# Performance work log

Hardware: AMD Instinct MI355X
Metric: run time of the kernel (lower is better)

The kernel has to match this reference:

```python
import jax, jax.numpy as jnp
import numpy as np

L, D, N = 4096, 1024, 16  # seq_len, d_model, hiddens_per_input


def setup_inputs() -> dict:
    key = jax.random.key(0)
    ks = jax.random.split(key, 9)
    x = jax.random.normal(ks[0], (L, D), dtype=jnp.float32)
    # Delta param (pre-softplus); softplus(Delta) > 0 is the discretization step
    Delta = jax.random.normal(ks[1], (D,), dtype=jnp.float32)
    # A stored as (re, im); default scheme uses A_re = -1 (stable), theta in [0, 2pi)
    A_re = -(0.5 + 0.5 * jax.random.uniform(ks[2], (D, N), dtype=jnp.float32))
    A_im = jax.random.uniform(ks[3], (D, N), dtype=jnp.float32) * 2.0 * jnp.pi
    scale = 1.0 / jnp.sqrt(jnp.float32(D))  # matrix_init: randn / sqrt(shape[0])
    B_re = jax.random.normal(ks[4], (D, N), dtype=jnp.float32) * scale
    B_im = jax.random.normal(ks[5], (D, N), dtype=jnp.float32) * scale
    C_re = jax.random.normal(ks[6], (D, N), dtype=jnp.float32) * scale
    C_im = jax.random.normal(ks[7], (D, N), dtype=jnp.float32) * scale
    D_param = jax.random.normal(ks[8], (D,), dtype=jnp.float32) * scale
    return {"x": x, "Delta": Delta, "A_re": A_re, "A_im": A_im,
            "B_re": B_re, "B_im": B_im, "C_re": C_re, "C_im": C_im,
            "D_param": D_param}


def _binary_operator_diag(q_i, q_j):
    """Associative op for diagonal linear recurrence h_j = A_j h_{j-1} + b_j."""
    A_i, b_i = q_i
    A_j, b_j = q_j
    return (A_j * A_i, A_j * b_i + b_j)


def reference(x, Delta, A_re, A_im, B_re, B_im, C_re, C_im, D_param):
    Bc = B_re + 1j * B_im                      # (D, N) complex
    Cc = C_re + 1j * C_im                      # (D, N) complex
    Ac = A_re + 1j * A_im                      # (D, N) complex
    dt = jax.nn.softplus(Delta)                # (D,)
    # shared_Delta=True branch: Lambda = exp(dt[:, None] * A), repeated over L
    Lam = jnp.exp(dt[:, None] * Ac)            # (D, N) complex
    Lambda_elements = jnp.broadcast_to(Lam[None, :, :], (x.shape[0], *Lam.shape))
    # Bu = einsum('D, D N, L D -> L D N', dt, B, x)
    Bu_elements = jnp.einsum('D,DN,LD->LDN', dt.astype(Bc.dtype), Bc,
                             x.astype(Bc.dtype))
    _, hidden_states = jax.lax.associative_scan(
        _binary_operator_diag, (Lambda_elements, Bu_elements))  # (L, D, N)
    out = jnp.einsum('LDN,DN->LD', hidden_states, Cc) + D_param[None, :] * x
    return out.real
```

## Files before the change

kernel.cpp:

```cpp
#include <hip/hip_runtime.h>
#include <math.h>

constexpr int L   = 4096;
constexpr int D   = 1024;
constexpr int CPB = 4;
constexpr int NB  = D / CPB;
constexpr int NCB = 128;
constexpr int T   = L / NCB;
constexpr int NT  = 1024;
constexpr int N   = 16;
constexpr int PAD = 65;

typedef float v2 __attribute__((ext_vector_type(2)));

__device__ __forceinline__ float softplus_f(float v) {
    return fmaxf(v, 0.0f) + log1pf(expf(-fabsf(v)));
}

__device__ __forceinline__ void lam_fast(float ar, float ai, float dt,
                                         float& lr, float& li) {
    float e = __expf(ar * dt);
    float s, c;
    __sincosf(ai * dt, &s, &c);
    lr = e * c;
    li = e * s;
}

__device__ __forceinline__ v2 vfma(v2 a, v2 b, v2 c) {
    return __builtin_elementwise_fma(a, b, c);
}

__global__ __launch_bounds__(NT, 4) void k_fused(
    const float* __restrict__ x,
    const float* __restrict__ Delta,
    const float* __restrict__ A_re, const float* __restrict__ A_im,
    const float* __restrict__ B_re, const float* __restrict__ B_im,
    const float* __restrict__ C_re, const float* __restrict__ C_im,
    const float* __restrict__ Dp,
    float* __restrict__ out)
{
    __shared__ float  xs[T * 512];
    __shared__ float2 sums[NCB * PAD];
    __shared__ float2 tot[16 * 64];

    const int b  = blockIdx.x;
    const int d0 = (b & 7) * 128 + (b >> 3) * 4;
    const int t  = threadIdx.x;

    const int h  = t & 1;
    const int dd = (t >> 1) & 3;
    const int ct = t >> 3;
    const int d  = d0 + dd;

    {
        const int rs = t & 7;
        float4 v[4];
        #pragma unroll
        for (int k = 0; k < 4; ++k) {
            int l = ct * T + rs * 4 + k;
            v[k] = *(const float4*)(x + (size_t)l * D + d0);
        }
        #pragma unroll
        for (int k = 0; k < 4; ++k)
            *(float4*)&xs[(rs * 4 + k) * 512 + ct * 4] = v[k];
    }

    const float dt = softplus_f(Delta[d]);

    v2 LR[4], LI[4];
    {
        const int base = d * N + h * 8;
        float4 a0 = *(const float4*)(A_re + base);
        float4 a1 = *(const float4*)(A_re + base + 4);
        float4 m0 = *(const float4*)(A_im + base);
        float4 m1 = *(const float4*)(A_im + base + 4);
        const float ar[8] = {a0.x, a0.y, a0.z, a0.w, a1.x, a1.y, a1.z, a1.w};
        const float ai[8] = {m0.x, m0.y, m0.z, m0.w, m1.x, m1.y, m1.z, m1.w};
        #pragma unroll
        for (int p = 0; p < 4; ++p) {
            float lr0, li0, lr1, li1;
            lam_fast(ar[2 * p], ai[2 * p], dt, lr0, li0);
            lam_fast(ar[2 * p + 1], ai[2 * p + 1], dt, lr1, li1);
            LR[p] = (v2){lr0, lr1};
            LI[p] = (v2){li0, li1};
        }
    }

    asm volatile("s_waitcnt vmcnt(0) lgkmcnt(0)" ::: "memory");

    v2 GR[4] = {(v2)0, (v2)0, (v2)0, (v2)0};
    v2 GI[4] = {(v2)0, (v2)0, (v2)0, (v2)0};
    #pragma unroll 4
    for (int i = 0; i < T; ++i) {
        float xv = xs[i * 512 + ct * 4 + dd];
        v2 XV = (v2){xv, xv};
        #pragma unroll
        for (int p = 0; p < 4; ++p) {
            v2 t2 = vfma(-LI[p], GI[p], XV);
            v2 nr = vfma(LR[p], GR[p], t2);
            GI[p] = vfma(LR[p], GI[p], LI[p] * GR[p]);
            GR[p] = nr;
        }
    }
    {
        float2* sp = &sums[ct * PAD + dd * 16 + h * 8];
        #pragma unroll
        for (int p = 0; p < 4; ++p) {
            sp[2 * p]     = make_float2(GR[p].x, GI[p].x);
            sp[2 * p + 1] = make_float2(GR[p].y, GI[p].y);
        }
    }

    const int lane = t & 63;
    const int w    = t >> 6;
    float l32r, l32i;
    {
        const int dd2 = lane >> 4, n2 = lane & 15;
        const int d2  = d0 + dd2;
        const float dt2 = softplus_f(Delta[d2]);
        lam_fast(A_re[d2 * N + n2], A_im[d2 * N + n2], dt2, l32r, l32i);
        #pragma unroll
        for (int k = 0; k < 5; ++k) {
            float nr = l32r * l32r - l32i * l32i;
            l32i = 2.0f * l32r * l32i;
            l32r = nr;
        }
    }

    asm volatile("s_waitcnt lgkmcnt(0)" ::: "memory");

    {
        float cr = 0.0f, ci = 0.0f;
        #pragma unroll
        for (int k = 0; k < 8; ++k) {
            const int idx = (w * 8 + k) * PAD + lane;
            float2 sv = sums[idx];
            sums[idx] = make_float2(cr, ci);
            float nr = fmaf(l32r, cr, fmaf(-l32i, ci, sv.x));
            ci = fmaf(l32r, ci, fmaf(l32i, cr, sv.y));
            cr = nr;
        }
        tot[w * 64 + lane] = make_float2(cr, ci);
    }

    float4 b0, b1, e0, e1, f0, f1, g0, g1;
    {
        const int base = d * N + h * 8;
        b0 = *(const float4*)(B_re + base);
        b1 = *(const float4*)(B_re + base + 4);
        e0 = *(const float4*)(B_im + base);
        e1 = *(const float4*)(B_im + base + 4);
        f0 = *(const float4*)(C_re + base);
        f1 = *(const float4*)(C_re + base + 4);
        g0 = *(const float4*)(C_im + base);
        g1 = *(const float4*)(C_im + base + 4);
    }
    const float dpv = Dp[d];

    __syncthreads();

    if (t < 64) {
        float rr = l32r, ri = l32i;
        #pragma unroll
        for (int k = 0; k < 3; ++k) {
            float nr = rr * rr - ri * ri;
            ri = 2.0f * rr * ri;
            rr = nr;
        }
        float cr = 0.0f, ci = 0.0f;
        #pragma unroll
        for (int u = 0; u < 16; ++u) {
            float2 sv = tot[u * 64 + t];
            tot[u * 64 + t] = make_float2(cr, ci);
            float nr = fmaf(rr, cr, fmaf(-ri, ci, sv.x));
            ci = fmaf(rr, ci, fmaf(ri, cr, sv.y));
            cr = nr;
        }
    }

    __syncthreads();

    {
        float2 g = tot[w * 64 + lane];
        float gr = g.x, gi = g.y;
        #pragma unroll
        for (int k = 0; k < 8; ++k) {
            const int idx = (w * 8 + k) * PAD + lane;
            float2 p = sums[idx];
            sums[idx] = make_float2(gr + p.x, gi + p.y);
            float nr = l32r * gr - l32i * gi;
            gi = fmaf(l32r, gi, l32i * gr);
            gr = nr;
        }
    }

    v2 CR[4], CI[4];
    {
        const float br[8] = {b0.x, b0.y, b0.z, b0.w, b1.x, b1.y, b1.z, b1.w};
        const float bi[8] = {e0.x, e0.y, e0.z, e0.w, e1.x, e1.y, e1.z, e1.w};
        const float cr[8] = {f0.x, f0.y, f0.z, f0.w, f1.x, f1.y, f1.z, f1.w};
        const float ci[8] = {g0.x, g0.y, g0.z, g0.w, g1.x, g1.y, g1.z, g1.w};
        #pragma unroll
        for (int p = 0; p < 4; ++p) {
            CR[p] = (v2){dt * (cr[2*p] * br[2*p] - ci[2*p] * bi[2*p]),
                         dt * (cr[2*p+1] * br[2*p+1] - ci[2*p+1] * bi[2*p+1])};
            CI[p] = (v2){dt * (cr[2*p] * bi[2*p] + ci[2*p] * br[2*p]),
                         dt * (cr[2*p+1] * bi[2*p+1] + ci[2*p+1] * br[2*p+1])};
        }
    }

    asm volatile("s_waitcnt lgkmcnt(0)" ::: "memory");

    {
        const float2* cp = &sums[ct * PAD + dd * 16 + h * 8];
        #pragma unroll
        for (int p = 0; p < 4; ++p) {
            float2 c0 = cp[2 * p], c1 = cp[2 * p + 1];
            GR[p] = (v2){c0.x, c1.x};
            GI[p] = (v2){c0.y, c1.y};
        }
    }
    const float dsel0 = h ? 0.0f : dpv;
    const float dsel1 = h ? dpv  : 0.0f;
    #pragma unroll
    for (int ob = 0; ob < T / 8; ++ob) {
        float P0[4], P1[4];
        #pragma unroll
        for (int ib = 0; ib < 4; ++ib) {
            #pragma unroll
            for (int u = 0; u < 2; ++u) {
                int i = ob * 8 + ib * 2 + u;
                float xv = xs[i * 512 + ct * 4 + dd];
                v2 XV = (v2){xv, xv};
                v2 ACC = (v2)0;
                #pragma unroll
                for (int p = 0; p < 4; ++p) {
                    v2 t2 = vfma(-LI[p], GI[p], XV);
                    v2 nr = vfma(LR[p], GR[p], t2);
                    GI[p] = vfma(LR[p], GI[p], LI[p] * GR[p]);
                    GR[p] = nr;
                    ACC = vfma(CR[p], GR[p], ACC);
                    ACC = vfma(-CI[p], GI[p], ACC);
                }
                float ap = ACC.x + ACC.y;
                ap = fmaf(u == 0 ? dsel0 : dsel1, xv, ap);
                if (u == 0) P0[ib] = ap; else P1[ib] = ap;
            }
        }
        float Vh[4];
        #pragma unroll
        for (int ib = 0; ib < 4; ++ib) {
            float mine  = h ? P1[ib] : P0[ib];
            float other = h ? P0[ib] : P1[ib];
            Vh[ib] = mine + __shfl_xor(other, 1);
        }
        float f[4];
        f[dd]     = Vh[dd];
        f[dd ^ 1] = __shfl_xor(Vh[dd ^ 1], 2);
        f[dd ^ 2] = __shfl_xor(Vh[dd ^ 2], 4);
        f[dd ^ 3] = __shfl_xor(Vh[dd ^ 3], 6);
        int row = ct * T + ob * 8 + dd * 2 + h;
        *(float4*)(out + (size_t)row * D + d0) =
            make_float4(f[0], f[1], f[2], f[3]);
    }
}

extern "C" void kernel_launch(void* const* d_in, const int* in_sizes, int n_in,
                              void* d_out, int out_size, void* d_ws, size_t ws_size,
                              hipStream_t stream) {
    const float* x     = (const float*)d_in[0];
    const float* Delta = (const float*)d_in[1];
    const float* A_re  = (const float*)d_in[2];
    const float* A_im  = (const float*)d_in[3];
    const float* B_re  = (const float*)d_in[4];
    const float* B_im  = (const float*)d_in[5];
    const float* C_re  = (const float*)d_in[6];
    const float* C_im  = (const float*)d_in[7];
    const float* Dp    = (const float*)d_in[8];
    float* out = (float*)d_out;

    k_fused<<<NB, NT, 0, stream>>>(x, Delta, A_re, A_im, B_re, B_im,
                                   C_re, C_im, Dp, out);
}
```

Baseline: 124.8 us.

## Split sequence into segments across blocks with cooperative grid sync for carries

```diff
diff --git a/kernel.cpp b/kernel.cpp
--- a/kernel.cpp
+++ b/kernel.cpp
@@ -1,15 +1,22 @@
 #include <hip/hip_runtime.h>
+#include <hip/hip_cooperative_groups.h>
 #include <math.h>
 
-constexpr int L   = 4096;
-constexpr int D   = 1024;
-constexpr int CPB = 4;
-constexpr int NB  = D / CPB;
-constexpr int NCB = 128;
-constexpr int T   = L / NCB;
-constexpr int NT  = 1024;
-constexpr int N   = 16;
-constexpr int PAD = 65;
+namespace cgrp = cooperative_groups;
+
+constexpr int L    = 4096;
+constexpr int D    = 1024;
+constexpr int N    = 16;
+constexpr int CPB  = 16;
+constexpr int NCG  = D / CPB;
+constexpr int NSEG = 4;
+constexpr int LSEG = L / NSEG;
+constexpr int NB   = NCG * NSEG;
+constexpr int NT   = 1024;
+constexpr int NCH  = 32;
+constexpr int T    = LSEG / NCH;
+constexpr int NST  = CPB * N;
+constexpr int SSTR = NST + 1;
 
 typedef float v2 __attribute__((ext_vector_type(2)));
 
@@ -37,34 +44,37 @@
     const float* __restrict__ B_re, const float* __restrict__ B_im,
     const float* __restrict__ C_re, const float* __restrict__ C_im,
     const float* __restrict__ Dp,
-    float* __restrict__ out)
+    float* __restrict__ out,
+    float2* __restrict__ sb, int two_sync)
 {
-    __shared__ float  xs[T * 512];
-    __shared__ float2 sums[NCB * PAD];
-    __shared__ float2 tot[16 * 64];
-
-    const int b  = blockIdx.x;
-    const int d0 = (b & 7) * 128 + (b >> 3) * 4;
-    const int t  = threadIdx.x;
+    __shared__ float  xs[LSEG * CPB];
+    __shared__ float2 sums[NCH * SSTR];
+    __shared__ float2 tot[4 * NST];
+
+    cgrp::grid_group grid = cgrp::this_grid();
+
+    const int blk = blockIdx.x;
+    const int cgi = blk & (NCG - 1);
+    const int seg = blk >> 6;
+    const int l0  = seg * LSEG;
+    const int c0  = cgi * CPB;
+    const int t   = threadIdx.x;
+
+    {
+        const int q = t & 3, r = t >> 2;
+        float4 v[4];
+        #pragma unroll
+        for (int k = 0; k < 4; ++k)
+            v[k] = *(const float4*)(x + (size_t)(l0 + r + 256 * k) * D + c0 + q * 4);
+        #pragma unroll
+        for (int k = 0; k < 4; ++k)
+            *(float4*)&xs[(r + 256 * k) * CPB + q * 4] = v[k];
+    }
 
     const int h  = t & 1;
-    const int dd = (t >> 1) & 3;
-    const int ct = t >> 3;
-    const int d  = d0 + dd;
-
-    {
-        const int rs = t & 7;
-        float4 v[4];
-        #pragma unroll
-        for (int k = 0; k < 4; ++k) {
-            int l = ct * T + rs * 4 + k;
-            v[k] = *(const float4*)(x + (size_t)l * D + d0);
-        }
-        #pragma unroll
-        for (int k = 0; k < 4; ++k)
-            *(float4*)&xs[(rs * 4 + k) * 512 + ct * 4] = v[k];
-    }
-
+    const int dd = (t >> 1) & 15;
+    const int ct = t >> 5;
+    const int d  = c0 + dd;
     const float dt = softplus_f(Delta[d]);
 
     v2 LR[4], LI[4];
@@ -85,14 +95,13 @@
             LI[p] = (v2){li0, li1};
         }
     }
-
-    asm volatile("s_waitcnt vmcnt(0) lgkmcnt(0)" ::: "memory");
+    __syncthreads();
 
     v2 GR[4] = {(v2)0, (v2)0, (v2)0, (v2)0};
     v2 GI[4] = {(v2)0, (v2)0, (v2)0, (v2)0};
     #pragma unroll 4
     for (int i = 0; i < T; ++i) {
-        float xv = xs[i * 512 + ct * 4 + dd];
+        float xv = xs[(ct * T + i) * CPB + dd];
         v2 XV = (v2){xv, xv};
         #pragma unroll
         for (int p = 0; p < 4; ++p) {
@@ -102,23 +111,24 @@
             GR[p] = nr;
         }
     }
-    {
-        float2* sp = &sums[ct * PAD + dd * 16 + h * 8];
-        #pragma unroll
-        for (int p = 0; p < 4; ++p) {
-            sp[2 * p]     = make_float2(GR[p].x, GI[p].x);
-            sp[2 * p + 1] = make_float2(GR[p].y, GI[p].y);
-        }
+    #pragma unroll
+    for (int p = 0; p < 4; ++p) {
+        const int s0 = (h * 8 + 2 * p) * CPB + dd;
+        sums[ct * SSTR + s0]       = make_float2(GR[p].x, GI[p].x);
+        sums[ct * SSTR + s0 + CPB] = make_float2(GR[p].y, GI[p].y);
     }
 
     const int lane = t & 63;
     const int w    = t >> 6;
+    const int SL   = w & 3;
+    const int WG   = w >> 2;
+    const int s    = SL * 64 + lane;
     float l32r, l32i;
     {
-        const int dd2 = lane >> 4, n2 = lane & 15;
-        const int d2  = d0 + dd2;
+        const int sdd = s & 15, sn = s >> 4;
+        const int d2 = c0 + sdd;
         const float dt2 = softplus_f(Delta[d2]);
-        lam_fast(A_re[d2 * N + n2], A_im[d2 * N + n2], dt2, l32r, l32i);
+        lam_fast(A_re[d2 * N + sn], A_im[d2 * N + sn], dt2, l32r, l32i);
         #pragma unroll
         for (int k = 0; k < 5; ++k) {
             float nr = l32r * l32r - l32i * l32i;
@@ -126,40 +136,39 @@
             l32r = nr;
         }
     }
-
-    asm volatile("s_waitcnt lgkmcnt(0)" ::: "memory");
+    __syncthreads();
 
     {
         float cr = 0.0f, ci = 0.0f;
         #pragma unroll
         for (int k = 0; k < 8; ++k) {
-            const int idx = (w * 8 + k) * PAD + lane;
+            const int idx = (WG * 8 + k) * SSTR + s;
             float2 sv = sums[idx];
             sums[idx] = make_float2(cr, ci);
             float nr = fmaf(l32r, cr, fmaf(-l32i, ci, sv.x));
             ci = fmaf(l32r, ci, fmaf(l32i, cr, sv.y));
             cr = nr;
         }
-        tot[w * 64 + lane] = make_float2(cr, ci);
-    }
-
-    float4 b0, b1, e0, e1, f0, f1, g0, g1;
+        tot[WG * NST + s] = make_float2(cr, ci);
+    }
+
+    float4 pb0, pb1, pe0, pe1, pf0, pf1, pg0, pg1;
     {
         const int base = d * N + h * 8;
-        b0 = *(const float4*)(B_re + base);
-        b1 = *(const float4*)(B_re + base + 4);
-        e0 = *(const float4*)(B_im + base);
-        e1 = *(const float4*)(B_im + base + 4);
-        f0 = *(const float4*)(C_re + base);
-        f1 = *(const float4*)(C_re + base + 4);
-        g0 = *(const float4*)(C_im + base);
-        g1 = *(const float4*)(C_im + base + 4);
+        pb0 = *(const float4*)(B_re + base);
+        pb1 = *(const float4*)(B_re + base + 4);
+        pe0 = *(const float4*)(B_im + base);
+        pe1 = *(const float4*)(B_im + base + 4);
+        pf0 = *(const float4*)(C_re + base);
+        pf1 = *(const float4*)(C_re + base + 4);
+        pg0 = *(const float4*)(C_im + base);
+        pg1 = *(const float4*)(C_im + base + 4);
     }
     const float dpv = Dp[d];
 
     __syncthreads();
 
-    if (t < 64) {
+    if (w < 4) {
         float rr = l32r, ri = l32i;
         #pragma unroll
         for (int k = 0; k < 3; ++k) {
@@ -169,37 +178,74 @@
         }
         float cr = 0.0f, ci = 0.0f;
         #pragma unroll
-        for (int u = 0; u < 16; ++u) {
-            float2 sv = tot[u * 64 + t];
-            tot[u * 64 + t] = make_float2(cr, ci);
+        for (int u = 0; u < 4; ++u) {
+            const int idx = u * NST + s;
+            float2 sv = tot[idx];
+            tot[idx] = make_float2(cr, ci);
             float nr = fmaf(rr, cr, fmaf(-ri, ci, sv.x));
             ci = fmaf(rr, ci, fmaf(ri, cr, sv.y));
             cr = nr;
         }
-    }
-
-    __syncthreads();
-
-    {
-        float2 g = tot[w * 64 + lane];
-        float gr = g.x, gi = g.y;
+        if (seg != NSEG - 1)
+            sb[(seg * NCG + cgi) * NST + s] = make_float2(cr, ci);
+    }
+    __syncthreads();
+    __threadfence();
+    grid.sync();
+    __threadfence();
+
+    float Cr = 0.0f, Ci = 0.0f;
+    if (seg > 0) {
+        float g1r = l32r, g1i = l32i;
+        #pragma unroll
+        for (int k = 0; k < 5; ++k) {
+            float nr = g1r * g1r - g1i * g1i;
+            g1i = 2.0f * g1r * g1i;
+            g1r = nr;
+        }
+        for (int j = 0; j < seg; ++j) {
+            float2 sv = sb[(j * NCG + cgi) * NST + s];
+            float nr = fmaf(g1r, Cr, fmaf(-g1i, Ci, sv.x));
+            Ci = fmaf(g1r, Ci, fmaf(g1i, Cr, sv.y));
+            Cr = nr;
+        }
+    }
+    if (two_sync) grid.sync();
+
+    {
+        float rr = l32r, ri = l32i;
+        #pragma unroll
+        for (int k = 0; k < 3; ++k) {
+            float nr = rr * rr - ri * ri;
+            ri = 2.0f * rr * ri;
+            rr = nr;
+        }
+        float pr = 1.0f, pi = 0.0f;
+        for (int k = 0; k < WG; ++k) {
+            float nr = pr * rr - pi * ri;
+            pi = fmaf(pr, ri, pi * rr);
+            pr = nr;
+        }
+        float2 g = tot[WG * NST + s];
+        float cr = fmaf(pr, Cr, fmaf(-pi, Ci, g.x));
+        float ci = fmaf(pr, Ci, fmaf(pi, Cr, g.y));
         #pragma unroll
         for (int k = 0; k < 8; ++k) {
-            const int idx = (w * 8 + k) * PAD + lane;
+            const int idx = (WG * 8 + k) * SSTR + s;
             float2 p = sums[idx];
-            sums[idx] = make_float2(gr + p.x, gi + p.y);
-            float nr = l32r * gr - l32i * gi;
-            gi = fmaf(l32r, gi, l32i * gr);
-            gr = nr;
+            sums[idx] = make_float2(cr + p.x, ci + p.y);
+            float nr = l32r * cr - l32i * ci;
+            ci = fmaf(l32r, ci, l32i * cr);
+            cr = nr;
         }
     }
 
     v2 CR[4], CI[4];
     {
-        const float br[8] = {b0.x, b0.y, b0.z, b0.w, b1.x, b1.y, b1.z, b1.w};
-        const float bi[8] = {e0.x, e0.y, e0.z, e0.w, e1.x, e1.y, e1.z, e1.w};
-        const float cr[8] = {f0.x, f0.y, f0.z, f0.w, f1.x, f1.y, f1.z, f1.w};
-        const float ci[8] = {g0.x, g0.y, g0.z, g0.w, g1.x, g1.y, g1.z, g1.w};
+        const float br[8] = {pb0.x, pb0.y, pb0.z, pb0.w, pb1.x, pb1.y, pb1.z, pb1.w};
+        const float bi[8] = {pe0.x, pe0.y, pe0.z, pe0.w, pe1.x, pe1.y, pe1.z, pe1.w};
+        const float cr[8] = {pf0.x, pf0.y, pf0.z, pf0.w, pf1.x, pf1.y, pf1.z, pf1.w};
+        const float ci[8] = {pg0.x, pg0.y, pg0.z, pg0.w, pg1.x, pg1.y, pg1.z, pg1.w};
         #pragma unroll
         for (int p = 0; p < 4; ++p) {
             CR[p] = (v2){dt * (cr[2*p] * br[2*p] - ci[2*p] * bi[2*p]),
@@ -208,20 +254,20 @@
                          dt * (cr[2*p+1] * bi[2*p+1] + ci[2*p+1] * br[2*p+1])};
         }
     }
-
-    asm volatile("s_waitcnt lgkmcnt(0)" ::: "memory");
-
-    {
-        const float2* cp = &sums[ct * PAD + dd * 16 + h * 8];
-        #pragma unroll
-        for (int p = 0; p < 4; ++p) {
-            float2 c0 = cp[2 * p], c1 = cp[2 * p + 1];
-            GR[p] = (v2){c0.x, c1.x};
-            GI[p] = (v2){c0.y, c1.y};
-        }
+    __syncthreads();
+
+    #pragma unroll
+    for (int p = 0; p < 4; ++p) {
+        const int s0 = (h * 8 + 2 * p) * CPB + dd;
+        float2 c0v = sums[ct * SSTR + s0];
+        float2 c1v = sums[ct * SSTR + s0 + CPB];
+        GR[p] = (v2){c0v.x, c1v.x};
+        GI[p] = (v2){c0v.y, c1v.y};
     }
     const float dsel0 = h ? 0.0f : dpv;
     const float dsel1 = h ? dpv  : 0.0f;
+    const int r0 = dd & 3;
+    const int cb = c0 + (dd >> 2) * 4;
     #pragma unroll
     for (int ob = 0; ob < T / 8; ++ob) {
         float P0[4], P1[4];
@@ -230,7 +276,7 @@
             #pragma unroll
             for (int u = 0; u < 2; ++u) {
                 int i = ob * 8 + ib * 2 + u;
-                float xv = xs[i * 512 + ct * 4 + dd];
+                float xv = xs[(ct * T + i) * CPB + dd];
                 v2 XV = (v2){xv, xv};
                 v2 ACC = (v2)0;
                 #pragma unroll
@@ -255,12 +301,12 @@
             Vh[ib] = mine + __shfl_xor(other, 1);
         }
         float f[4];
-        f[dd]     = Vh[dd];
-        f[dd ^ 1] = __shfl_xor(Vh[dd ^ 1], 2);
-        f[dd ^ 2] = __shfl_xor(Vh[dd ^ 2], 4);
-        f[dd ^ 3] = __shfl_xor(Vh[dd ^ 3], 6);
-        int row = ct * T + ob * 8 + dd * 2 + h;
-        *(float4*)(out + (size_t)row * D + d0) =
+        f[r0]     = Vh[r0];
+        f[r0 ^ 1] = __shfl_xor(Vh[r0 ^ 1], 2);
+        f[r0 ^ 2] = __shfl_xor(Vh[r0 ^ 2], 4);
+        f[r0 ^ 3] = __shfl_xor(Vh[r0 ^ 3], 6);
+        int row = l0 + ct * T + ob * 8 + r0 * 2 + h;
+        *(float4*)(out + (size_t)row * D + cb) =
             make_float4(f[0], f[1], f[2], f[3]);
     }
 }
@@ -279,6 +325,18 @@
     const float* Dp    = (const float*)d_in[8];
     float* out = (float*)d_out;
 
-    k_fused<<<NB, NT, 0, stream>>>(x, Delta, A_re, A_im, B_re, B_im,
-                                   C_re, C_im, Dp, out);
-}
+    const size_t need = sizeof(float2) * (size_t)NSEG * NCG * NST;
+    float2* sb;
+    int two_sync;
+    if (d_ws != nullptr && ws_size >= need) {
+        sb = (float2*)d_ws;  two_sync = 0;
+    } else {
+        sb = (float2*)d_out; two_sync = 1;
+    }
+
+    void* args[] = {(void*)&x, (void*)&Delta, (void*)&A_re, (void*)&A_im,
+                    (void*)&B_re, (void*)&B_im, (void*)&C_re, (void*)&C_im,
+                    (void*)&Dp, (void*)&out, (void*)&sb, (void*)&two_sync};
+    hipLaunchCooperativeKernel((const void*)k_fused, dim3(NB), dim3(NT),
+                               args, 0, stream);
+}
```

New measurement: 281.8 us. 2.26x slower.
